# Kernel tuning notes

Measured on AMD Instinct MI355X. Metric: run time of the kernel, lower is better.

Reference implementation:

```python
import jax, jax.numpy as jnp
import numpy as np

NUM_EMBEDDINGS = 1024
EMBEDDING_DIM = 256
COMMITMENT_COST = 0.25
DECAY = 0.99
EPS = 1e-5


def setup_inputs() -> dict:
    key = jax.random.key(0)
    k0, k1, k2 = jax.random.split(key, 3)
    x = jax.random.normal(k0, (32, 2048, EMBEDDING_DIM), dtype=jnp.float32)
    # embedding.weight.data.uniform_(-1/K, 1/K)
    embedding_w = jax.random.uniform(
        k1, (NUM_EMBEDDINGS, EMBEDDING_DIM), dtype=jnp.float32,
        minval=-1.0 / NUM_EMBEDDINGS, maxval=1.0 / NUM_EMBEDDINGS)
    ema_cluster_size = jnp.zeros((NUM_EMBEDDINGS,), dtype=jnp.float32)
    ema_w = jax.random.normal(k2, (NUM_EMBEDDINGS, EMBEDDING_DIM), dtype=jnp.float32)
    return {"x": x, "embedding_w": embedding_w,
            "ema_cluster_size": ema_cluster_size, "ema_w": ema_w}


def reference(x, embedding_w, ema_cluster_size, ema_w):
    K, D = embedding_w.shape
    flat = x.reshape(-1, D)  # [N, D]

    # squared L2 distances to codebook: [N, K]
    distances = ((flat * flat).sum(axis=1, keepdims=True)
                 - 2.0 * flat @ embedding_w.T
                 + (embedding_w * embedding_w).sum(axis=1))
    indices = jnp.argmin(distances, axis=1)  # [N] int

    # gather quantized vectors
    quantized = embedding_w[indices].reshape(x.shape)

    # EMA statistics via scatter-add (one-hot.T @ flat without materializing one-hot)
    counts = jax.ops.segment_sum(jnp.ones((flat.shape[0],), dtype=flat.dtype),
                                 indices, num_segments=K)  # [K]
    dw = jax.ops.segment_sum(flat, indices, num_segments=K)  # [K, D]

    new_cluster_size = DECAY * ema_cluster_size + (1.0 - DECAY) * counts
    new_ema_w = DECAY * ema_w + (1.0 - DECAY) * dw

    # Laplace smoothing of cluster sizes, normalized codebook update
    n = new_cluster_size.sum()
    cs = (new_cluster_size + EPS) / (n + K * EPS) * n
    new_embedding_w = new_ema_w / cs[:, None]

    # commitment loss (codebook side is EMA-updated, so only e-latent term)
    e_latent_loss = jnp.mean((jax.lax.stop_gradient(quantized) - x) ** 2)
    loss = COMMITMENT_COST * e_latent_loss

    # straight-through estimator
    quantized_st = x + jax.lax.stop_gradient(quantized - x)

    avg_probs = counts / counts.sum()
    perplexity = jnp.exp(-jnp.sum(avg_probs * jnp.log(avg_probs + 1e-10)))

    return (loss, quantized_st, perplexity,
            new_embedding_w, new_cluster_size, new_ema_w)
```

## Files before the change

### kernel.cpp

```cpp
#include <hip/hip_runtime.h>
#include <math.h>

#define N_ROWS   65536
#define K_EMB    1024
#define D_EMB    256

typedef __attribute__((ext_vector_type(8)))  short short8;
typedef __attribute__((ext_vector_type(4)))  short short4v;
typedef __attribute__((ext_vector_type(16))) float floatx16;

__device__ inline unsigned short f2bf(float f) {
    unsigned u = __float_as_uint(f);
    unsigned r = u + 0x7fffu + ((u >> 16) & 1u);
    return (unsigned short)(r >> 16);
}
__device__ inline float bf2f(unsigned short s) {
    return __uint_as_float(((unsigned)s) << 16);
}

__global__ __launch_bounds__(64)
void prep_e(const float* __restrict__ ew, float* __restrict__ half_esq,
            short* __restrict__ pack_hi, short* __restrict__ pack_lo)
{
    const int k = blockIdx.x;
    const int t = threadIdx.x;
    float4 v = *(const float4*)(ew + (size_t)k * D_EMB + t * 4);
    float s = v.x * v.x + v.y * v.y + v.z * v.z + v.w * v.w;
#pragma unroll
    for (int off = 32; off > 0; off >>= 1) s += __shfl_down(s, off);
    if (t == 0) half_esq[k] = 0.5f * s;

    const int d0   = t * 4;
    const int tile = k >> 5;
    const int kt   = d0 >> 4;
    const int half = (d0 & 15) >> 3;
    const int lane = (k & 31) + 32 * half;
    const int j0   = d0 & 7;
    const int off  = tile * 8192 + kt * 512 + lane * 8 + j0;

    float f[4] = {-v.x, -v.y, -v.z, -v.w};
    short4v h, l;
#pragma unroll
    for (int j = 0; j < 4; ++j) {
        unsigned short hh = f2bf(f[j]);
        h[j] = (short)hh;
        l[j] = (short)f2bf(f[j] - bf2f(hh));
    }
    *(short4v*)(pack_hi + off) = h;
    *(short4v*)(pack_lo + off) = l;
}

__global__ __launch_bounds__(256, 2)
void argmin_mfma(const float* __restrict__ x,
                 const short* __restrict__ pack_hi,
                 const short* __restrict__ pack_lo,
                 const float* __restrict__ half_esq,
                 const float* __restrict__ ew,
                 int* __restrict__ indices,
                 float* __restrict__ out_q,
                 double* __restrict__ loss_buckets)
{
    __shared__ short xs_hi[32 * 256];
    __shared__ short xs_lo[32 * 256];
    __shared__ float cmv[128];
    __shared__ int   cmi[128];
    __shared__ int   widx[32];

    const int t  = threadIdx.x;
    const int r0 = blockIdx.x * 32;

#pragma unroll
    for (int i = 0; i < 4; ++i) {
        int q   = i * 256 + t;
        int row = q >> 5;
        int g8  = q & 31;
        const float* gp = x + (size_t)(r0 + row) * D_EMB + g8 * 8;
        float4 a = *(const float4*)gp;
        float4 b = *(const float4*)(gp + 4);
        float f[8] = {a.x, a.y, a.z, a.w, b.x, b.y, b.z, b.w};
        short8 h8, l8;
#pragma unroll
        for (int j = 0; j < 8; ++j) {
            unsigned short hh = f2bf(f[j]);
            h8[j] = (short)hh;
            l8[j] = (short)f2bf(f[j] - bf2f(hh));
        }
        int off = row * 256 + ((g8 ^ (row & 7)) << 3);
        *(short8*)(xs_hi + off) = h8;
        *(short8*)(xs_lo + off) = l8;
    }
    __syncthreads();

    const int w    = t >> 6;
    const int lane = t & 63;
    const int l31  = lane & 31;
    const int half = lane >> 5;
    const int key  = l31 & 7;
    const short* bbase_h = xs_hi + l31 * 256;
    const short* bbase_l = xs_lo + l31 * 256;

    float mv = 3.4e38f;
    int   mi = 0;

    for (int cp = 0; cp < 4; ++cp) {
        const int c0 = w * 256 + cp * 64;
        const int c1 = c0 + 32;
        const int tile0 = c0 >> 5;

        floatx16 acc0, acc1;
#pragma unroll
        for (int rq = 0; rq < 4; ++rq) {
            float4 e0 = *(const float4*)(half_esq + c0 + rq * 8 + half * 4);
            float4 e1 = *(const float4*)(half_esq + c1 + rq * 8 + half * 4);
            acc0[rq * 4 + 0] = e0.x; acc0[rq * 4 + 1] = e0.y;
            acc0[rq * 4 + 2] = e0.z; acc0[rq * 4 + 3] = e0.w;
            acc1[rq * 4 + 0] = e1.x; acc1[rq * 4 + 1] = e1.y;
            acc1[rq * 4 + 2] = e1.z; acc1[rq * 4 + 3] = e1.w;
        }

        const short* p0h = pack_hi + tile0 * 8192 + lane * 8;
        const short* p0l = pack_lo + tile0 * 8192 + lane * 8;
        const short* p1h = p0h + 8192;
        const short* p1l = p0l + 8192;

        short8 a0h = *(const short8*)(p0h);
        short8 a0l = *(const short8*)(p0l);
        short8 a1h = *(const short8*)(p1h);
        short8 a1l = *(const short8*)(p1l);

#pragma unroll 4
        for (int kt = 0; kt < 16; ++kt) {
            short8 n0h, n0l, n1h, n1l;
            if (kt < 15) {
                n0h = *(const short8*)(p0h + (kt + 1) * 512);
                n0l = *(const short8*)(p0l + (kt + 1) * 512);
                n1h = *(const short8*)(p1h + (kt + 1) * 512);
                n1l = *(const short8*)(p1l + (kt + 1) * 512);
            }
            int coff = (((2 * kt + half) ^ key) << 3);
            short8 bh = *(const short8*)(bbase_h + coff);
            short8 bl = *(const short8*)(bbase_l + coff);
            acc0 = __builtin_amdgcn_mfma_f32_32x32x16_bf16(a0h, bh, acc0, 0, 0, 0);
            acc1 = __builtin_amdgcn_mfma_f32_32x32x16_bf16(a1h, bh, acc1, 0, 0, 0);
            acc0 = __builtin_amdgcn_mfma_f32_32x32x16_bf16(a0h, bl, acc0, 0, 0, 0);
            acc1 = __builtin_amdgcn_mfma_f32_32x32x16_bf16(a1h, bl, acc1, 0, 0, 0);
            acc0 = __builtin_amdgcn_mfma_f32_32x32x16_bf16(a0l, bh, acc0, 0, 0, 0);
            acc1 = __builtin_amdgcn_mfma_f32_32x32x16_bf16(a1l, bh, acc1, 0, 0, 0);
            a0h = n0h; a0l = n0l; a1h = n1h; a1l = n1l;
        }

#pragma unroll
        for (int r = 0; r < 16; ++r) {
            int code0 = c0 + (r & 3) + ((r >> 2) << 3) + half * 4;
            float v0 = acc0[r];
            if (v0 < mv || (v0 == mv && code0 < mi)) { mv = v0; mi = code0; }
            int code1 = code0 + 32;
            float v1 = acc1[r];
            if (v1 < mv || (v1 == mv && code1 < mi)) { mv = v1; mi = code1; }
        }
    }

    {
        float ov = __shfl_xor(mv, 32);
        int   oi = __shfl_xor(mi, 32);
        if (ov < mv || (ov == mv && oi < mi)) { mv = ov; mi = oi; }
    }

    if (half == 0) {
        int slot = w * 32 + l31;
        cmv[slot] = mv;
        cmi[slot] = mi;
    }
    __syncthreads();
    if (t < 32) {
        float bv = cmv[t];
        int   bi = cmi[t];
#pragma unroll
        for (int ww = 1; ww < 4; ++ww) {
            float v = cmv[ww * 32 + t];
            int   i = cmi[ww * 32 + t];
            if (v < bv || (v == bv && i < bi)) { bv = v; bi = i; }
        }
        indices[r0 + t] = bi;
        widx[t] = bi;
    }
    __syncthreads();

    const int g8e  = lane >> 1;
    const int j0e  = (lane & 1) * 4;
    float lsum = 0.0f;
#pragma unroll
    for (int rr = 0; rr < 8; ++rr) {
        const int row = w * 8 + rr;
        const int idx = widx[row];
        const int off = row * 256 + (((g8e) ^ (row & 7)) << 3) + j0e;
        short4v h4 = *(const short4v*)(xs_hi + off);
        short4v l4 = *(const short4v*)(xs_lo + off);
        float xr[4];
#pragma unroll
        for (int j = 0; j < 4; ++j)
            xr[j] = bf2f((unsigned short)h4[j]) + bf2f((unsigned short)l4[j]);
        const float4 ev = *(const float4*)(ew + (size_t)idx * D_EMB + lane * 4);
        float4 q;
        q.x = xr[0] + (ev.x - xr[0]);
        q.y = xr[1] + (ev.y - xr[1]);
        q.z = xr[2] + (ev.z - xr[2]);
        q.w = xr[3] + (ev.w - xr[3]);
        *(float4*)(out_q + (size_t)(r0 + row) * D_EMB + lane * 4) = q;
        float dx = ev.x - xr[0], dy = ev.y - xr[1];
        float dz = ev.z - xr[2], dwv = ev.w - xr[3];
        lsum += dx * dx + dy * dy + dz * dz + dwv * dwv;
    }
#pragma unroll
    for (int off = 32; off > 0; off >>= 1) lsum += __shfl_down(lsum, off);
    if (lane == 0) atomicAdd(&loss_buckets[blockIdx.x & 255], (double)lsum);
}

__global__ __launch_bounds__(256)
void code_stats(const float* __restrict__ x,
                const int* __restrict__ indices,
                float* __restrict__ dw,
                int* __restrict__ counts)
{
    __shared__ int rows[2048];
    __shared__ int nmatch;
    const int k    = blockIdx.x >> 2;
    const int sl   = blockIdx.x & 3;
    const int t    = threadIdx.x;
    const int rbeg = sl * (N_ROWS / 4);
    float sum = 0.0f;
    int total = 0;

    for (int c = 0; c < N_ROWS / 4; c += 2048) {
        if (t == 0) nmatch = 0;
        __syncthreads();
        const int base = rbeg + c + t * 8;
        int4 a = *(const int4*)(indices + base);
        int4 b = *(const int4*)(indices + base + 4);
        int m[8] = {a.x, a.y, a.z, a.w, b.x, b.y, b.z, b.w};
#pragma unroll
        for (int j = 0; j < 8; ++j)
            if (m[j] == k) { int p = atomicAdd(&nmatch, 1); rows[p] = base + j; }
        __syncthreads();
        const int n = nmatch;
        total += n;
        for (int r = 0; r < n; ++r)
            sum += x[(size_t)rows[r] * D_EMB + t];
        __syncthreads();
    }
    if (total > 0) {
        atomicAdd(&dw[(size_t)k * D_EMB + t], sum);
        if (t == 0) atomicAdd(&counts[k], total);
    }
}

__global__ __launch_bounds__(1024)
void finalize_small(const float* __restrict__ ema_cs,
                    const int* __restrict__ counts,
                    const double* __restrict__ loss_buckets,
                    float* __restrict__ cs_ws,
                    float* __restrict__ out_loss,
                    float* __restrict__ out_perp,
                    float* __restrict__ out_ncs)
{
    __shared__ float  red[1024];
    __shared__ double redd[256];
    const int k = threadIdx.x;
    const float cnt = (float)counts[k];
    const float ncs = 0.99f * ema_cs[k] + 0.01f * cnt;
    out_ncs[k] = ncs;
    red[k] = ncs;
    __syncthreads();
    for (int off = 512; off > 0; off >>= 1) {
        if (k < off) red[k] += red[k + off];
        __syncthreads();
    }
    const float n = red[0];
    __syncthreads();
    cs_ws[k] = (ncs + 1e-5f) / (n + 1024.0f * 1e-5f) * n;

    const float p = cnt / 65536.0f;
    red[k] = p * logf(p + 1e-10f);
    if (k < 256) redd[k] = loss_buckets[k];
    __syncthreads();
    for (int off = 512; off > 0; off >>= 1) {
        if (k < off) red[k] += red[k + off];
        __syncthreads();
    }
    if (k == 0) out_perp[0] = expf(-red[0]);
    for (int off = 128; off > 0; off >>= 1) {
        if (k < off) redd[k] += redd[k + off];
        __syncthreads();
    }
    if (k == 0) out_loss[0] = (float)(0.25 * (redd[0] / 16777216.0));
}

__global__ __launch_bounds__(256)
void codebook_kernel(const float* __restrict__ ema_w,
                     const float* __restrict__ dw,
                     const float* __restrict__ cs_ws,
                     float* __restrict__ out_emb,
                     float* __restrict__ out_ema)
{
    const int k = blockIdx.x;
    const int d = threadIdx.x;
    const size_t o = (size_t)k * D_EMB + d;
    const float nev = 0.99f * ema_w[o] + 0.01f * dw[o];
    out_ema[o] = nev;
    out_emb[o] = nev / cs_ws[k];
}

extern "C" void kernel_launch(void* const* d_in, const int* in_sizes, int n_in,
                              void* d_out, int out_size, void* d_ws, size_t ws_size,
                              hipStream_t stream)
{
    const float* x       = (const float*)d_in[0];
    const float* ew      = (const float*)d_in[1];
    const float* ema_cs  = (const float*)d_in[2];
    const float* ema_w   = (const float*)d_in[3];

    float* out       = (float*)d_out;
    float* out_loss  = out;
    float* out_q     = out + 1;
    float* out_perp  = out + 1 + 16777216;
    float* out_emb   = out_perp + 1;
    float* out_ncs   = out_emb + 262144;
    float* out_ema   = out_ncs + 1024;

    char* ws = (char*)d_ws;
    float*  dw           = (float*)(ws);
    int*    counts       = (int*)(ws + 1048576);
    double* loss_buckets = (double*)(ws + 1052672);
    float*  half_esq     = (float*)(ws + 1054720);
    float*  cs_ws        = (float*)(ws + 1058816);
    int*    indices      = (int*)(ws + 1062912);

    short* pack_hi = (short*)(out + 16777220);
    short* pack_lo = (short*)(out + 16777220 + 131072);

    hipMemsetAsync(ws, 0, 1054720, stream);

    prep_e<<<K_EMB, 64, 0, stream>>>(ew, half_esq, pack_hi, pack_lo);
    argmin_mfma<<<N_ROWS / 32, 256, 0, stream>>>(x, pack_hi, pack_lo, half_esq,
                                                 ew, indices, out_q, loss_buckets);
    code_stats<<<K_EMB * 4, 256, 0, stream>>>(x, indices, dw, counts);
    finalize_small<<<1, 1024, 0, stream>>>(ema_cs, counts, loss_buckets, cs_ws,
                                           out_loss, out_perp, out_ncs);
    codebook_kernel<<<K_EMB, 256, 0, stream>>>(ema_w, dw, cs_ws, out_emb, out_ema);
}
```

Before: 270.0 us.

## Replace per-code index scan with counting-sort bucketing for EMA segment sums

Cluster counts are now built with atomics inside the argmin kernel. A prefix scan in the finalize kernel produces per-code offsets, and a scatter kernel writes row ids grouped by code. Each code's block then gathers only its own rows to form dw and writes the codebook update directly, fused with the former codebook kernel. This removes the old code_stats pass, where 4096 blocks each scanned the whole index array, and it also drops the large memset and the dw atomics. In exchange it adds two small launches, and the summation order becomes atomic-order dependent and therefore nondeterministic.

```diff
diff --git a/kernel.cpp b/kernel.cpp
--- a/kernel.cpp
+++ b/kernel.cpp
@@ -20,10 +20,17 @@
 
 __global__ __launch_bounds__(64)
 void prep_e(const float* __restrict__ ew, float* __restrict__ half_esq,
-            short* __restrict__ pack_hi, short* __restrict__ pack_lo)
+            short* __restrict__ pack_hi, short* __restrict__ pack_lo,
+            int* __restrict__ counts, double* __restrict__ loss_buckets)
 {
     const int k = blockIdx.x;
     const int t = threadIdx.x;
+
+    if (t == 0) {
+        counts[k] = 0;
+        if (k < 256) loss_buckets[k] = 0.0;
+    }
+
     float4 v = *(const float4*)(ew + (size_t)k * D_EMB + t * 4);
     float s = v.x * v.x + v.y * v.y + v.z * v.z + v.w * v.w;
 #pragma unroll
@@ -58,7 +65,8 @@
                  const float* __restrict__ ew,
                  int* __restrict__ indices,
                  float* __restrict__ out_q,
-                 double* __restrict__ loss_buckets)
+                 double* __restrict__ loss_buckets,
+                 int* __restrict__ counts)
 {
     __shared__ short xs_hi[32 * 256];
     __shared__ short xs_lo[32 * 256];
@@ -183,6 +191,7 @@
         }
         indices[r0 + t] = bi;
         widx[t] = bi;
+        atomicAdd(&counts[bi], 1);
     }
     __syncthreads();
 
@@ -216,44 +225,6 @@
     if (lane == 0) atomicAdd(&loss_buckets[blockIdx.x & 255], (double)lsum);
 }
 
-__global__ __launch_bounds__(256)
-void code_stats(const float* __restrict__ x,
-                const int* __restrict__ indices,
-                float* __restrict__ dw,
-                int* __restrict__ counts)
-{
-    __shared__ int rows[2048];
-    __shared__ int nmatch;
-    const int k    = blockIdx.x >> 2;
-    const int sl   = blockIdx.x & 3;
-    const int t    = threadIdx.x;
-    const int rbeg = sl * (N_ROWS / 4);
-    float sum = 0.0f;
-    int total = 0;
-
-    for (int c = 0; c < N_ROWS / 4; c += 2048) {
-        if (t == 0) nmatch = 0;
-        __syncthreads();
-        const int base = rbeg + c + t * 8;
-        int4 a = *(const int4*)(indices + base);
-        int4 b = *(const int4*)(indices + base + 4);
-        int m[8] = {a.x, a.y, a.z, a.w, b.x, b.y, b.z, b.w};
-#pragma unroll
-        for (int j = 0; j < 8; ++j)
-            if (m[j] == k) { int p = atomicAdd(&nmatch, 1); rows[p] = base + j; }
-        __syncthreads();
-        const int n = nmatch;
-        total += n;
-        for (int r = 0; r < n; ++r)
-            sum += x[(size_t)rows[r] * D_EMB + t];
-        __syncthreads();
-    }
-    if (total > 0) {
-        atomicAdd(&dw[(size_t)k * D_EMB + t], sum);
-        if (t == 0) atomicAdd(&counts[k], total);
-    }
-}
-
 __global__ __launch_bounds__(1024)
 void finalize_small(const float* __restrict__ ema_cs,
                     const int* __restrict__ counts,
@@ -261,15 +232,20 @@
                     float* __restrict__ cs_ws,
                     float* __restrict__ out_loss,
                     float* __restrict__ out_perp,
-                    float* __restrict__ out_ncs)
+                    float* __restrict__ out_ncs,
+                    int* __restrict__ offsets,
+                    int* __restrict__ cursor)
 {
     __shared__ float  red[1024];
     __shared__ double redd[256];
+    __shared__ int    sc[1024];
     const int k = threadIdx.x;
-    const float cnt = (float)counts[k];
+    const int icnt = counts[k];
+    const float cnt = (float)icnt;
     const float ncs = 0.99f * ema_cs[k] + 0.01f * cnt;
     out_ncs[k] = ncs;
     red[k] = ncs;
+    sc[k]  = icnt;
     __syncthreads();
     for (int off = 512; off > 0; off >>= 1) {
         if (k < off) red[k] += red[k + off];
@@ -278,6 +254,15 @@
     const float n = red[0];
     __syncthreads();
     cs_ws[k] = (ncs + 1e-5f) / (n + 1024.0f * 1e-5f) * n;
+
+    for (int d = 1; d < 1024; d <<= 1) {
+        int add = (k >= d) ? sc[k - d] : 0;
+        __syncthreads();
+        sc[k] += add;
+        __syncthreads();
+    }
+    offsets[k] = sc[k] - icnt;
+    cursor[k]  = 0;
 
     const float p = cnt / 65536.0f;
     red[k] = p * logf(p + 1e-10f);
@@ -296,16 +281,54 @@
 }
 
 __global__ __launch_bounds__(256)
-void codebook_kernel(const float* __restrict__ ema_w,
-                     const float* __restrict__ dw,
-                     const float* __restrict__ cs_ws,
-                     float* __restrict__ out_emb,
-                     float* __restrict__ out_ema)
-{
-    const int k = blockIdx.x;
-    const int d = threadIdx.x;
-    const size_t o = (size_t)k * D_EMB + d;
-    const float nev = 0.99f * ema_w[o] + 0.01f * dw[o];
+void scatter_rows(const int* __restrict__ indices,
+                  const int* __restrict__ offsets,
+                  int* __restrict__ cursor,
+                  int* __restrict__ row_sorted)
+{
+    const int row = blockIdx.x * 256 + threadIdx.x;
+    const int idx = indices[row];
+    const int pos = atomicAdd(&cursor[idx], 1);
+    row_sorted[offsets[idx] + pos] = row;
+}
+
+__global__ __launch_bounds__(256)
+void gather_update(const float* __restrict__ x,
+                   const int* __restrict__ row_sorted,
+                   const int* __restrict__ offsets,
+                   const int* __restrict__ counts,
+                   const float* __restrict__ ema_w,
+                   const float* __restrict__ cs_ws,
+                   float* __restrict__ out_emb,
+                   float* __restrict__ out_ema)
+{
+    __shared__ int rows[2048];
+    const int k   = blockIdx.x;
+    const int t   = threadIdx.x;
+    const int off = offsets[k];
+    const int cnt = counts[k];
+    float sum = 0.0f;
+
+    for (int c = 0; c < cnt; c += 2048) {
+        const int m = min(cnt - c, 2048);
+        for (int i = t; i < m; i += 256) rows[i] = row_sorted[off + c + i];
+        __syncthreads();
+        int r = 0;
+        for (; r + 4 <= m; r += 4) {
+            int i0 = rows[r], i1 = rows[r + 1], i2 = rows[r + 2], i3 = rows[r + 3];
+            float v0 = x[(size_t)i0 * D_EMB + t];
+            float v1 = x[(size_t)i1 * D_EMB + t];
+            float v2 = x[(size_t)i2 * D_EMB + t];
+            float v3 = x[(size_t)i3 * D_EMB + t];
+            sum += (v0 + v1) + (v2 + v3);
+        }
+        for (; r < m; ++r)
+            sum += x[(size_t)rows[r] * D_EMB + t];
+        __syncthreads();
+    }
+
+    const size_t o = (size_t)k * D_EMB + t;
+    const float nev = 0.99f * ema_w[o] + 0.01f * sum;
     out_ema[o] = nev;
     out_emb[o] = nev / cs_ws[k];
 }
@@ -328,23 +351,28 @@
     float* out_ema   = out_ncs + 1024;
 
     char* ws = (char*)d_ws;
-    float*  dw           = (float*)(ws);
-    int*    counts       = (int*)(ws + 1048576);
-    double* loss_buckets = (double*)(ws + 1052672);
-    float*  half_esq     = (float*)(ws + 1054720);
-    float*  cs_ws        = (float*)(ws + 1058816);
-    int*    indices      = (int*)(ws + 1062912);
+    int*    counts       = (int*)(ws);
+    double* loss_buckets = (double*)(ws + 4096);
+    float*  half_esq     = (float*)(ws + 6144);
+    float*  cs_ws        = (float*)(ws + 10240);
+    int*    offsets      = (int*)(ws + 14336);
+    int*    cursor       = (int*)(ws + 18432);
+    int*    indices      = (int*)(ws + 22528);
+    int*    row_sorted   = (int*)(ws + 284672);
 
     short* pack_hi = (short*)(out + 16777220);
     short* pack_lo = (short*)(out + 16777220 + 131072);
 
-    hipMemsetAsync(ws, 0, 1054720, stream);
-
-    prep_e<<<K_EMB, 64, 0, stream>>>(ew, half_esq, pack_hi, pack_lo);
+    prep_e<<<K_EMB, 64, 0, stream>>>(ew, half_esq, pack_hi, pack_lo,
+                                     counts, loss_buckets);
     argmin_mfma<<<N_ROWS / 32, 256, 0, stream>>>(x, pack_hi, pack_lo, half_esq,
-                                                 ew, indices, out_q, loss_buckets);
-    code_stats<<<K_EMB * 4, 256, 0, stream>>>(x, indices, dw, counts);
+                                                 ew, indices, out_q, loss_buckets,
+                                                 counts);
     finalize_small<<<1, 1024, 0, stream>>>(ema_cs, counts, loss_buckets, cs_ws,
-                                           out_loss, out_perp, out_ncs);
-    codebook_kernel<<<K_EMB, 256, 0, stream>>>(ema_w, dw, cs_ws, out_emb, out_ema);
-}
+                                           out_loss, out_perp, out_ncs,
+                                           offsets, cursor);
+    scatter_rows<<<N_ROWS / 256, 256, 0, stream>>>(indices, offsets, cursor,
+                                                   row_sorted);
+    gather_update<<<K_EMB, 256, 0, stream>>>(x, row_sorted, offsets, counts,
+                                             ema_w, cs_ws, out_emb, out_ema);
+}
```

Result: faster. 264.4 us (-2.1%).
